# Optimization experiments

Hardware: AMD Instinct MI355X
Metric: run time of the kernel (lower is better)

The kernel has to match this reference:

```python
import jax, jax.numpy as jnp
import numpy as np

C = 512
NUM_HEADS = 8


def setup_inputs() -> dict:
    key = jax.random.key(0)
    k1, k2, k3 = jax.random.split(key, 3)
    x = jax.random.normal(k1, (16, C, 32, 32), dtype=jnp.float32)
    # torch Linear(C, 3C) weight shape [3C, C]; y = x @ W.T
    w_qkv = jax.random.normal(k2, (3 * C, C), dtype=jnp.float32) * (1.0 / np.sqrt(C))
    w_out = jax.random.normal(k3, (C, C), dtype=jnp.float32) * (1.0 / np.sqrt(C))
    return {"x": x, "w_qkv": w_qkv, "w_out": w_out}


def reference(x, w_qkv, w_out):
    B, Cc, H, W = x.shape
    S = H * W
    hd = Cc // NUM_HEADS
    # NCHW -> (B, S, C)
    xs = jnp.transpose(x, (0, 2, 3, 1)).reshape(B, S, Cc)
    qkv = jnp.einsum('bsc,dc->bsd', xs, w_qkv).reshape(B, S, 3, NUM_HEADS, hd)
    q = jnp.transpose(qkv[:, :, 0], (0, 2, 1, 3))  # (B, h, S, hd)
    k = jnp.transpose(qkv[:, :, 1], (0, 2, 1, 3))
    v = jnp.transpose(qkv[:, :, 2], (0, 2, 1, 3))
    scale = 1.0 / np.sqrt(hd)
    logits = jnp.einsum('bhqd,bhkd->bhqk', q, k) * scale
    attn = jax.nn.softmax(logits, axis=-1)
    o = jnp.einsum('bhqk,bhkd->bhqd', attn, v)  # (B, h, S, hd)
    o = jnp.transpose(o, (0, 2, 1, 3)).reshape(B, S, Cc)
    out = jnp.einsum('bsc,dc->bsd', o, w_out)
    return jnp.transpose(out.reshape(B, H, W, Cc), (0, 3, 1, 2))
```

## Files before the change

kernel.cpp:

```cpp
#include <hip/hip_runtime.h>
#include <hip/hip_bf16.h>
#include <stdint.h>


typedef __bf16 bf16x8 __attribute__((ext_vector_type(8)));
typedef __bf16 bf16x4 __attribute__((ext_vector_type(4)));
typedef float  f32x4  __attribute__((ext_vector_type(4)));
typedef short  s16x4  __attribute__((ext_vector_type(4)));

#if __has_builtin(__builtin_amdgcn_exp2f)
#define EXP2(x) __builtin_amdgcn_exp2f(x)
#else
#define EXP2(x) exp2f(x)
#endif

#define GLDS16(gptr, lptr)                                                        \
  __builtin_amdgcn_global_load_lds(                                               \
      (const __attribute__((address_space(1))) uint32_t*)(gptr),                  \
      (__attribute__((address_space(3))) uint32_t*)(lptr), 16, 0, 0)

__global__ __launch_bounds__(256) void k_transpose_x(const float* __restrict__ x,
                                                     __bf16* __restrict__ xs) {
  __shared__ float tl[64][36];
  const int s0 = blockIdx.x * 32, c0 = blockIdx.y * 64, b = blockIdx.z;
  const int t = threadIdx.x;
  const int cl = t >> 2, f0 = (t & 3) * 2;
#pragma unroll
  for (int i = 0; i < 2; ++i) {
    const float4 v = *reinterpret_cast<const float4*>(
        x + ((size_t)(b * 512 + c0 + cl)) * 1024 + s0 + (f0 + i) * 4);
    *reinterpret_cast<float4*>(&tl[cl][(f0 + i) * 4]) = v;
  }
  __syncthreads();
  const int sl = t >> 3, ch = t & 7;
  bf16x8 o;
#pragma unroll
  for (int j = 0; j < 8; ++j) o[j] = (__bf16)tl[ch * 8 + j][sl];
  *reinterpret_cast<bf16x8*>(xs + ((size_t)(b * 1024 + s0 + sl)) * 512 + c0 + ch * 8) = o;
}

__global__ __launch_bounds__(256) void k_cast4(const float* __restrict__ in,
                                               __bf16* __restrict__ out) {
  const int i = blockIdx.x * 256 + threadIdx.x;
  const float4 v = reinterpret_cast<const float4*>(in)[i];
  bf16x4 o = {(__bf16)v.x, (__bf16)v.y, (__bf16)v.z, (__bf16)v.w};
  reinterpret_cast<bf16x4*>(out)[i] = o;
}

__device__ __forceinline__ void gemm_core(const __bf16* __restrict__ Ag,
                                          const __bf16* __restrict__ Bg,
                                          int m0, int n0,
                                          __bf16* As, __bf16* Bs,
                                          f32x4 (&acc)[4][4]) {
  const int tid = threadIdx.x, lane = tid & 63, wv = tid >> 6;
  const int wm = (wv >> 1) * 64, wn = (wv & 1) * 64;
  const int lr = lane & 15, lq = lane >> 4;
  const int srow8 = lane >> 3, sc = lane & 7;
  for (int k0 = 0; k0 < 512; k0 += 64) {
    __syncthreads();
#pragma unroll
    for (int t = 0; t < 4; ++t) {
      const int r0 = (wv * 4 + t) * 8;
      const int row = r0 + srow8;
      const int gc = ((sc ^ (row & 7)) * 8);
      GLDS16(Ag + (size_t)(m0 + row) * 512 + k0 + gc, &As[r0 * 64]);
      GLDS16(Bg + (size_t)(n0 + row) * 512 + k0 + gc, &Bs[r0 * 64]);
    }
    __syncthreads();
#pragma unroll
    for (int kk = 0; kk < 64; kk += 32) {
      bf16x8 af[4], bfr[4];
#pragma unroll
      for (int i = 0; i < 4; ++i) {
        const int row = wm + i * 16 + lr;
        af[i] = *reinterpret_cast<const bf16x8*>(
            &As[row * 64 + ((((kk >> 3) + lq) ^ (lr & 7)) * 8)]);
      }
#pragma unroll
      for (int j = 0; j < 4; ++j) {
        const int row = wn + j * 16 + lr;
        bfr[j] = *reinterpret_cast<const bf16x8*>(
            &Bs[row * 64 + ((((kk >> 3) + lq) ^ (lr & 7)) * 8)]);
      }
#pragma unroll
      for (int i = 0; i < 4; ++i)
#pragma unroll
        for (int j = 0; j < 4; ++j)
          acc[i][j] = __builtin_amdgcn_mfma_f32_16x16x32_bf16(af[i], bfr[j], acc[i][j], 0, 0, 0);
    }
  }
}

__global__ __launch_bounds__(256) void k_qkv_gemm(const __bf16* __restrict__ xs,
                                                  const __bf16* __restrict__ wq,
                                                  __bf16* __restrict__ Q,
                                                  __bf16* __restrict__ K,
                                                  __bf16* __restrict__ Vt) {
  __shared__ __align__(16) __bf16 As[128 * 64];
  __shared__ __align__(16) __bf16 Bs[128 * 64];
  const int m0 = blockIdx.x * 128, n0 = blockIdx.y * 128;
  const int tid = threadIdx.x, lane = tid & 63, wv = tid >> 6;
  const int wm = (wv >> 1) * 64, wn = (wv & 1) * 64;
  const int lr = lane & 15, lq = lane >> 4;
  f32x4 acc[4][4] = {};
  gemm_core(xs, wq, m0, n0, As, Bs, acc);
  const float QSC = 0.125f * 1.44269504088896341f;
#pragma unroll
  for (int i = 0; i < 4; ++i) {
    const int mg0 = m0 + wm + i * 16 + lq * 4;
    const int b = mg0 >> 10, s = mg0 & 1023;
#pragma unroll
    for (int j = 0; j < 4; ++j) {
      const int ng = n0 + wn + j * 16 + lr;
      const int t = ng >> 9, h = (ng >> 6) & 7, d = ng & 63;
      if (t == 0) {
#pragma unroll
        for (int r = 0; r < 4; ++r)
          Q[((size_t)((b * 8 + h) * 1024 + s + r)) * 64 + d] = (__bf16)(acc[i][j][r] * QSC);
      } else if (t == 1) {
#pragma unroll
        for (int r = 0; r < 4; ++r)
          K[((size_t)((b * 8 + h) * 1024 + s + r)) * 64 + d] = (__bf16)acc[i][j][r];
      } else {
        bf16x4 pv = {(__bf16)acc[i][j][0], (__bf16)acc[i][j][1],
                     (__bf16)acc[i][j][2], (__bf16)acc[i][j][3]};
        *reinterpret_cast<bf16x4*>(&Vt[((size_t)((b * 8 + h) * 64 + d)) * 1024 + s]) = pv;
      }
    }
  }
}

__global__ __launch_bounds__(256, 4) void k_attn(const __bf16* __restrict__ Q,
                                                 const __bf16* __restrict__ K,
                                                 const __bf16* __restrict__ Vt,
                                                 __bf16* __restrict__ O) {
  __shared__ __align__(16) __bf16 Ks[2][64 * 64];
  __shared__ __align__(16) __bf16 Vs[2][64 * 64];
  const int qt = blockIdx.x, h = blockIdx.y, b = blockIdx.z;
  const int tid = threadIdx.x, lane = tid & 63, wv = tid >> 6;
  const int lr = lane & 15, lq = lane >> 4;
  const size_t hbase = (size_t)(b * 8 + h) * 65536;

  bf16x8 qb[2][2];
#pragma unroll
  for (int g = 0; g < 2; ++g)
#pragma unroll
    for (int kx = 0; kx < 2; ++kx)
      qb[g][kx] = *reinterpret_cast<const bf16x8*>(
          Q + hbase + (size_t)(qt * 128 + wv * 32 + g * 16 + lr) * 64 + kx * 32 + lq * 8);

  const int srow8 = lane >> 3, sc = lane & 7;
  int srow[2], sgc[2];
#pragma unroll
  for (int t = 0; t < 2; ++t) {
    srow[t] = wv * 16 + t * 8 + srow8;
    sgc[t] = ((sc ^ (srow[t] & 7)) * 8);
  }
#define STAGE(kt, buf)                                                             \
  {                                                                                \
    _Pragma("unroll") for (int t = 0; t < 2; ++t) {                                \
      const int r0 = wv * 16 + t * 8;                                              \
      GLDS16(K + hbase + (size_t)((kt) * 64 + srow[t]) * 64 + sgc[t],              \
             &Ks[buf][r0 * 64]);                                                   \
      GLDS16(Vt + hbase + (size_t)srow[t] * 1024 + (kt) * 64 + sgc[t],             \
             &Vs[buf][r0 * 64]);                                                   \
    }                                                                              \
  }

  float l_run[2] = {0.f, 0.f};
  f32x4 o_acc[2][4] = {};

  STAGE(0, 0);
  __syncthreads();

#pragma unroll 2
  for (int kt = 0; kt < 16; ++kt) {
    const int cur = kt & 1;
    if (kt < 15) STAGE(kt + 1, cur ^ 1);
    f32x4 sacc[2][4] = {};
#pragma unroll
    for (int kx = 0; kx < 2; ++kx)
#pragma unroll
      for (int jt = 0; jt < 4; ++jt) {
        const int row = jt * 16 + lr;
        const bf16x8 ka = *reinterpret_cast<const bf16x8*>(
            &Ks[cur][row * 64 + (((kx * 4 + lq) ^ (lr & 7)) * 8)]);
        sacc[0][jt] = __builtin_amdgcn_mfma_f32_16x16x32_bf16(ka, qb[0][kx], sacc[0][jt], 0, 0, 0);
        sacc[1][jt] = __builtin_amdgcn_mfma_f32_16x16x32_bf16(ka, qb[1][kx], sacc[1][jt], 0, 0, 0);
      }
    s16x4 pb[2][4];
#pragma unroll
    for (int g = 0; g < 2; ++g) {
      float ls = 0.f;
#pragma unroll
      for (int c = 0; c < 4; ++c) {
        const float p0 = EXP2(sacc[g][c][0]);
        const float p1 = EXP2(sacc[g][c][1]);
        const float p2 = EXP2(sacc[g][c][2]);
        const float p3 = EXP2(sacc[g][c][3]);
        ls += (p0 + p1) + (p2 + p3);
        bf16x4 pv = {(__bf16)p0, (__bf16)p1, (__bf16)p2, (__bf16)p3};
        pb[g][c] = __builtin_bit_cast(s16x4, pv);
      }
      l_run[g] += ls;
    }
#pragma unroll
    for (int c = 0; c < 4; ++c)
#pragma unroll
      for (int dt = 0; dt < 4; ++dt) {
        const int d = dt * 16 + lr;
        const s16x4 va = *reinterpret_cast<const s16x4*>(
            &Vs[cur][d * 64 + (((2 * c + (lq >> 1)) ^ (lr & 7)) * 8) + (lq & 1) * 4]);
        o_acc[0][dt] = __builtin_amdgcn_mfma_f32_16x16x16bf16_1k(va, pb[0][c], o_acc[0][dt], 0, 0, 0);
        o_acc[1][dt] = __builtin_amdgcn_mfma_f32_16x16x16bf16_1k(va, pb[1][c], o_acc[1][dt], 0, 0, 0);
      }
    __syncthreads();
  }
#pragma unroll
  for (int g = 0; g < 2; ++g) {
    float l1 = l_run[g] + __shfl_xor(l_run[g], 16, 64);
    const float inv = 1.0f / (l1 + __shfl_xor(l1, 32, 64));
    const int sg = qt * 128 + wv * 32 + g * 16 + lr;
#pragma unroll
    for (int dt = 0; dt < 4; ++dt) {
      const int c0 = h * 64 + dt * 16 + lq * 4;
      bf16x4 ov = {(__bf16)(o_acc[g][dt][0] * inv), (__bf16)(o_acc[g][dt][1] * inv),
                   (__bf16)(o_acc[g][dt][2] * inv), (__bf16)(o_acc[g][dt][3] * inv)};
      *reinterpret_cast<bf16x4*>(&O[((size_t)(b * 1024 + sg)) * 512 + c0]) = ov;
    }
  }
}

__global__ __launch_bounds__(256) void k_out_gemm(const __bf16* __restrict__ wo,
                                                  const __bf16* __restrict__ Ob,
                                                  float* __restrict__ out) {
  __shared__ __align__(16) __bf16 As[128 * 64];
  __shared__ __align__(16) __bf16 Bs[128 * 64];
  const int n0 = blockIdx.x * 128, m0 = blockIdx.y * 128;
  const int tid = threadIdx.x, lane = tid & 63, wv = tid >> 6;
  const int wm = (wv >> 1) * 64, wn = (wv & 1) * 64;
  const int lr = lane & 15, lq = lane >> 4;
  f32x4 acc[4][4] = {};
  gemm_core(wo, Ob, m0, n0, As, Bs, acc);
  const int b = n0 >> 10;
#pragma unroll
  for (int i = 0; i < 4; ++i) {
    const int cch = m0 + wm + i * 16 + lq * 4;
#pragma unroll
    for (int j = 0; j < 4; ++j) {
      const int s = (n0 & 1023) + wn + j * 16 + lr;
#pragma unroll
      for (int r = 0; r < 4; ++r)
        out[((size_t)(b * 512 + cch + r)) * 1024 + s] = acc[i][j][r];
    }
  }
}

extern "C" void kernel_launch(void* const* d_in, const int* in_sizes, int n_in,
                              void* d_out, int out_size, void* d_ws, size_t ws_size,
                              hipStream_t stream) {
  const float* x    = (const float*)d_in[0];
  const float* wqkv = (const float*)d_in[1];
  const float* wout = (const float*)d_in[2];
  float* out = (float*)d_out;
  char* ws = (char*)d_ws;
  __bf16* xs    = (__bf16*)(ws);
  __bf16* wqkvb = (__bf16*)(ws + 16777216);
  __bf16* woutb = (__bf16*)(ws + 18350080);
  __bf16* Qb    = (__bf16*)(ws + 18874368);
  __bf16* Kb    = (__bf16*)(ws + 35651584);
  __bf16* Vtb   = (__bf16*)(ws + 52428800);
  __bf16* Ob    = (__bf16*)(ws + 69206016);

  k_transpose_x<<<dim3(32, 8, 16), dim3(256), 0, stream>>>(x, xs);
  k_cast4<<<dim3(768), dim3(256), 0, stream>>>(wqkv, wqkvb);
  k_cast4<<<dim3(256), dim3(256), 0, stream>>>(wout, woutb);
  k_qkv_gemm<<<dim3(128, 12), dim3(256), 0, stream>>>(xs, wqkvb, Qb, Kb, Vtb);
  k_attn<<<dim3(8, 8, 16), dim3(256), 0, stream>>>(Qb, Kb, Vtb, Ob);
  k_out_gemm<<<dim3(128, 4), dim3(256), 0, stream>>>(woutb, Ob, out);
}
```

Before: 203.0 us.

## Double-buffer GEMM LDS tiles with BK=32 and merge weight-cast launches

The shared GEMM core now double-buffers LDS with a 32-wide K step, prefetching the next tile through global_load_lds while MFMAs run on the current one. This replaces the old two-barrier single-buffer loop, and the XOR swizzle is adjusted to the narrower tile. Both GEMMs get a launch-bounds occupancy hint of 4, and the two weight-cast kernels are merged into one launch. The cost is twice as many loop iterations and one barrier per 32-wide K step. The correctness of the prefetch relies on the single end-of-iteration barrier.

```diff
diff --git a/kernel.cpp b/kernel.cpp
--- a/kernel.cpp
+++ b/kernel.cpp
@@ -39,9 +39,14 @@
   *reinterpret_cast<bf16x8*>(xs + ((size_t)(b * 1024 + s0 + sl)) * 512 + c0 + ch * 8) = o;
 }
 
-__global__ __launch_bounds__(256) void k_cast4(const float* __restrict__ in,
-                                               __bf16* __restrict__ out) {
-  const int i = blockIdx.x * 256 + threadIdx.x;
+__global__ __launch_bounds__(256) void k_cast_w(const float* __restrict__ wqkv,
+                                                const float* __restrict__ wout,
+                                                __bf16* __restrict__ wqkvb,
+                                                __bf16* __restrict__ woutb) {
+  const int blk = blockIdx.x;
+  const float* in = (blk < 768) ? wqkv : wout;
+  __bf16* out = (blk < 768) ? wqkvb : woutb;
+  const int i = ((blk < 768) ? blk : blk - 768) * 256 + threadIdx.x;
   const float4 v = reinterpret_cast<const float4*>(in)[i];
   bf16x4 o = {(__bf16)v.x, (__bf16)v.y, (__bf16)v.z, (__bf16)v.w};
   reinterpret_cast<bf16x4*>(out)[i] = o;
@@ -55,49 +60,55 @@
   const int tid = threadIdx.x, lane = tid & 63, wv = tid >> 6;
   const int wm = (wv >> 1) * 64, wn = (wv & 1) * 64;
   const int lr = lane & 15, lq = lane >> 4;
-  const int srow8 = lane >> 3, sc = lane & 7;
-  for (int k0 = 0; k0 < 512; k0 += 64) {
+  const int srl = lane >> 2, pc = lane & 3;
+  const int gcs = ((pc ^ (srl & 3)) * 8);
+
+#define GSTAGE(k0s, buf)                                                           \
+  {                                                                                \
+    _Pragma("unroll") for (int t = 0; t < 2; ++t) {                                \
+      const int r0 = wv * 32 + t * 16;                                             \
+      const int sr = r0 + srl;                                                     \
+      GLDS16(Ag + (size_t)(m0 + sr) * 512 + (k0s) + gcs, &As[(buf) * 4096 + r0 * 32]); \
+      GLDS16(Bg + (size_t)(n0 + sr) * 512 + (k0s) + gcs, &Bs[(buf) * 4096 + r0 * 32]); \
+    }                                                                              \
+  }
+
+  GSTAGE(0, 0);
+  __syncthreads();
+#pragma unroll 2
+  for (int k0 = 0; k0 < 512; k0 += 32) {
+    const int cur = (k0 >> 5) & 1;
+    if (k0 < 480) GSTAGE(k0 + 32, cur ^ 1);
+    bf16x8 af[4], bfr[4];
+#pragma unroll
+    for (int i = 0; i < 4; ++i) {
+      const int row = wm + i * 16 + lr;
+      af[i] = *reinterpret_cast<const bf16x8*>(
+          &As[cur * 4096 + row * 32 + ((lq ^ (lr & 3)) * 8)]);
+    }
+#pragma unroll
+    for (int j = 0; j < 4; ++j) {
+      const int row = wn + j * 16 + lr;
+      bfr[j] = *reinterpret_cast<const bf16x8*>(
+          &Bs[cur * 4096 + row * 32 + ((lq ^ (lr & 3)) * 8)]);
+    }
+#pragma unroll
+    for (int i = 0; i < 4; ++i)
+#pragma unroll
+      for (int j = 0; j < 4; ++j)
+        acc[i][j] = __builtin_amdgcn_mfma_f32_16x16x32_bf16(af[i], bfr[j], acc[i][j], 0, 0, 0);
     __syncthreads();
-#pragma unroll
-    for (int t = 0; t < 4; ++t) {
-      const int r0 = (wv * 4 + t) * 8;
-      const int row = r0 + srow8;
-      const int gc = ((sc ^ (row & 7)) * 8);
-      GLDS16(Ag + (size_t)(m0 + row) * 512 + k0 + gc, &As[r0 * 64]);
-      GLDS16(Bg + (size_t)(n0 + row) * 512 + k0 + gc, &Bs[r0 * 64]);
-    }
-    __syncthreads();
-#pragma unroll
-    for (int kk = 0; kk < 64; kk += 32) {
-      bf16x8 af[4], bfr[4];
-#pragma unroll
-      for (int i = 0; i < 4; ++i) {
-        const int row = wm + i * 16 + lr;
-        af[i] = *reinterpret_cast<const bf16x8*>(
-            &As[row * 64 + ((((kk >> 3) + lq) ^ (lr & 7)) * 8)]);
-      }
-#pragma unroll
-      for (int j = 0; j < 4; ++j) {
-        const int row = wn + j * 16 + lr;
-        bfr[j] = *reinterpret_cast<const bf16x8*>(
-            &Bs[row * 64 + ((((kk >> 3) + lq) ^ (lr & 7)) * 8)]);
-      }
-#pragma unroll
-      for (int i = 0; i < 4; ++i)
-#pragma unroll
-        for (int j = 0; j < 4; ++j)
-          acc[i][j] = __builtin_amdgcn_mfma_f32_16x16x32_bf16(af[i], bfr[j], acc[i][j], 0, 0, 0);
-    }
-  }
-}
-
-__global__ __launch_bounds__(256) void k_qkv_gemm(const __bf16* __restrict__ xs,
-                                                  const __bf16* __restrict__ wq,
-                                                  __bf16* __restrict__ Q,
-                                                  __bf16* __restrict__ K,
-                                                  __bf16* __restrict__ Vt) {
-  __shared__ __align__(16) __bf16 As[128 * 64];
-  __shared__ __align__(16) __bf16 Bs[128 * 64];
+  }
+#undef GSTAGE
+}
+
+__global__ __launch_bounds__(256, 4) void k_qkv_gemm(const __bf16* __restrict__ xs,
+                                                     const __bf16* __restrict__ wq,
+                                                     __bf16* __restrict__ Q,
+                                                     __bf16* __restrict__ K,
+                                                     __bf16* __restrict__ Vt) {
+  __shared__ __align__(16) __bf16 As[2 * 128 * 32];
+  __shared__ __align__(16) __bf16 Bs[2 * 128 * 32];
   const int m0 = blockIdx.x * 128, n0 = blockIdx.y * 128;
   const int tid = threadIdx.x, lane = tid & 63, wv = tid >> 6;
   const int wm = (wv >> 1) * 64, wn = (wv & 1) * 64;
@@ -231,11 +242,11 @@
   }
 }
 
-__global__ __launch_bounds__(256) void k_out_gemm(const __bf16* __restrict__ wo,
-                                                  const __bf16* __restrict__ Ob,
-                                                  float* __restrict__ out) {
-  __shared__ __align__(16) __bf16 As[128 * 64];
-  __shared__ __align__(16) __bf16 Bs[128 * 64];
+__global__ __launch_bounds__(256, 4) void k_out_gemm(const __bf16* __restrict__ wo,
+                                                     const __bf16* __restrict__ Ob,
+                                                     float* __restrict__ out) {
+  __shared__ __align__(16) __bf16 As[2 * 128 * 32];
+  __shared__ __align__(16) __bf16 Bs[2 * 128 * 32];
   const int n0 = blockIdx.x * 128, m0 = blockIdx.y * 128;
   const int tid = threadIdx.x, lane = tid & 63, wv = tid >> 6;
   const int wm = (wv >> 1) * 64, wn = (wv & 1) * 64;
@@ -273,8 +284,7 @@
   __bf16* Ob    = (__bf16*)(ws + 69206016);
 
   k_transpose_x<<<dim3(32, 8, 16), dim3(256), 0, stream>>>(x, xs);
-  k_cast4<<<dim3(768), dim3(256), 0, stream>>>(wqkv, wqkvb);
-  k_cast4<<<dim3(256), dim3(256), 0, stream>>>(wout, woutb);
+  k_cast_w<<<dim3(1024), dim3(256), 0, stream>>>(wqkv, wout, wqkvb, woutb);
   k_qkv_gemm<<<dim3(128, 12), dim3(256), 0, stream>>>(xs, wqkvb, Qb, Kb, Vtb);
   k_attn<<<dim3(8, 8, 16), dim3(256), 0, stream>>>(Qb, Kb, Vtb, Ob);
   k_out_gemm<<<dim3(128, 4), dim3(256), 0, stream>>>(woutb, Ob, out);
```

After: 202.3 us. Within noise of the previous version (-0.3%).
